# Kernel tuning notes

Hardware: AMD Instinct MI355X
Metric: run time of the kernel (lower is better)

The kernel has to match this reference:

```python
import jax, jax.numpy as jnp
import numpy as np

H = 16  # num_heads

def setup_inputs() -> dict:
    key = jax.random.key(0)
    k1, k2, k3 = jax.random.split(key, 3)
    D = 1024
    x = jax.random.normal(k1, (4, 2048, D), dtype=jnp.float32)
    W_qkv = jax.random.normal(k2, (D, 3 * D), dtype=jnp.float32) * (1.0 / np.sqrt(D))
    b_qkv = jnp.zeros((3 * D,), dtype=jnp.float32)
    W_out = jax.random.normal(k3, (D, D), dtype=jnp.float32) * (1.0 / np.sqrt(D))
    b_out = jnp.zeros((D,), dtype=jnp.float32)
    return {"x": x, "W_qkv": W_qkv, "b_qkv": b_qkv, "W_out": W_out, "b_out": b_out}

def reference(x, W_qkv, b_qkv, W_out, b_out):
    B, S, D = x.shape
    hd = D // H  # head_dim
    qkv = x @ W_qkv + b_qkv  # [B,S,3D]
    q, k, v = jnp.split(qkv, 3, axis=-1)
    # [B,S,D] -> [B,H,S,hd]
    q = q.reshape(B, S, H, hd).transpose(0, 2, 1, 3)
    k = k.reshape(B, S, H, hd).transpose(0, 2, 1, 3)
    v = v.reshape(B, S, H, hd).transpose(0, 2, 1, 3)
    scores = jnp.einsum('bhqd,bhkd->bhqk', q, k) / jnp.sqrt(jnp.float32(hd))
    weights = jax.nn.softmax(scores, axis=-1)  # dropout p=0.0 (eval)
    out = jnp.einsum('bhqk,bhkd->bhqd', weights, v)
    out = out.transpose(0, 2, 1, 3).reshape(B, S, D)
    return out @ W_out + b_out
```

## Files before the change

kernel.cpp:

```cpp
#include <hip/hip_runtime.h>

typedef __bf16 bf16;
typedef __bf16 bf16x8 __attribute__((ext_vector_type(8)));
typedef float f32x4 __attribute__((ext_vector_type(4)));
typedef unsigned u32x2 __attribute__((ext_vector_type(2)));

static constexpr int NB = 4;
static constexpr int NS = 2048;
static constexpr int ND = 1024;
static constexpr int NH = 16;
static constexpr int HD = 64;
static constexpr float QSCALE = 0.18033688011112042f;

#define GL16(g, l)                                                             \
    __builtin_amdgcn_global_load_lds(                                          \
        (const __attribute__((address_space(1))) void*)(g),                    \
        (__attribute__((address_space(3))) void*)(l), 16, 0, 0)

static __device__ __forceinline__ unsigned pk2(float a, float b) {
    union { __bf16 h[2]; unsigned u; } t;
    t.h[0] = (__bf16)a; t.h[1] = (__bf16)b;
    return t.u;
}

__global__ void k_conv(const float* __restrict__ in, bf16* __restrict__ out, int n) {
    int i = (blockIdx.x * blockDim.x + threadIdx.x) * 4;
    if (i < n) {
        float4 v = *reinterpret_cast<const float4*>(in + i);
        bf16* o = out + i;
        o[0] = (bf16)v.x; o[1] = (bf16)v.y; o[2] = (bf16)v.z; o[3] = (bf16)v.w;
    }
}

__global__ void k_transconv(const float* __restrict__ in, bf16* __restrict__ out,
                            int K, int N) {
    __shared__ float tile[32][33];
    int k0 = blockIdx.y * 32, n0 = blockIdx.x * 32;
    int tx = threadIdx.x, ty = threadIdx.y;
    for (int j = 0; j < 32; j += 8)
        tile[ty + j][tx] = in[(long)(k0 + ty + j) * N + n0 + tx];
    __syncthreads();
    for (int j = 0; j < 32; j += 8)
        out[(long)(n0 + ty + j) * K + k0 + tx] = (bf16)tile[tx][ty + j];
}

template <int EPI>
__global__ __launch_bounds__(256, 2) void k_gemm(
    const bf16* __restrict__ A, const bf16* __restrict__ Bt,
    const float* __restrict__ bias,
    void* __restrict__ out0, void* __restrict__ out1, void* __restrict__ out2,
    int M, int N, int Kd)
{
    constexpr int BM = 128, BN = 128, BK = 64;
    __shared__ __align__(16) bf16 As[2][BM * BK];
    __shared__ __align__(16) bf16 Bs[2][BN * BK];

    const int t = threadIdx.x;
    const int wid = t >> 6, lane = t & 63;
    const int wm = wid >> 1, wn = wid & 1;
    const int m0 = blockIdx.y * BM, n0 = blockIdx.x * BN;
    const int lrow = lane & 15, lhi = lane >> 4;

    const int srow0 = wid * 32 + (lane >> 3);
    const int scol = ((lane & 7) ^ (lane >> 3)) * 8;
    const bf16* ag = A + (long)(m0 + srow0) * Kd + scol;
    const bf16* bg = Bt + (long)(n0 + srow0) * Kd + scol;

    auto STAGE = [&](int buf_, int k0_) {
#pragma unroll
        for (int c = 0; c < 4; ++c) {
            GL16(ag + (long)(c * 8) * Kd + k0_, &As[buf_][(wid * 32 + c * 8) * BK]);
            GL16(bg + (long)(c * 8) * Kd + k0_, &Bs[buf_][(wid * 32 + c * 8) * BK]);
        }
    };

    f32x4 acc[4][4] = {};
    const int nt = Kd >> 6;
    const int swzr = (lrow & 7) << 4;
    int co[2];
#pragma unroll
    for (int kk = 0; kk < 2; ++kk)
        co[kk] = ((kk * 64 + lhi * 16) ^ swzr) >> 1;

    STAGE(0, 0);
    int cur = 0;
    for (int tix = 0; tix < nt; ++tix) {
        if (tix + 1 < nt) {
            STAGE(cur ^ 1, (tix + 1) * BK);
            asm volatile("s_waitcnt vmcnt(8)" ::: "memory");
        } else {
            asm volatile("s_waitcnt vmcnt(0)" ::: "memory");
        }
        __builtin_amdgcn_s_barrier();
        __builtin_amdgcn_sched_barrier(0);

        bf16x8 af[2][4], bfr[2][4];
#pragma unroll
        for (int kk = 0; kk < 2; ++kk)
#pragma unroll
            for (int i = 0; i < 4; ++i) {
                af[kk][i]  = *reinterpret_cast<const bf16x8*>(
                    &As[cur][(wm * 64 + i * 16 + lrow) * BK + co[kk]]);
                bfr[kk][i] = *reinterpret_cast<const bf16x8*>(
                    &Bs[cur][(wn * 64 + i * 16 + lrow) * BK + co[kk]]);
            }
        __builtin_amdgcn_s_setprio(1);
#pragma unroll
        for (int kk = 0; kk < 2; ++kk)
#pragma unroll
            for (int i = 0; i < 4; ++i)
#pragma unroll
                for (int j = 0; j < 4; ++j)
                    acc[i][j] = __builtin_amdgcn_mfma_f32_16x16x32_bf16(
                        af[kk][i], bfr[kk][j], acc[i][j], 0, 0, 0);
        __builtin_amdgcn_s_setprio(0);
        __builtin_amdgcn_s_barrier();
        cur ^= 1;
    }

    if (EPI == 0) {
        bf16* Qb = (bf16*)out0; bf16* Kb = (bf16*)out1; bf16* Vt = (bf16*)out2;
#pragma unroll
        for (int j = 0; j < 4; ++j) {
            int col = n0 + wn * 64 + j * 16 + lrow;
            float bv = bias[col];
            int which = col >> 10;
            int rem = col & 1023;
            int h = rem >> 6, d = rem & 63;
#pragma unroll
            for (int i = 0; i < 4; ++i) {
                int mbase = m0 + wm * 64 + i * 16 + lhi * 4;
#pragma unroll
                for (int r = 0; r < 4; ++r) {
                    int row = mbase + r;
                    int bb = row >> 11, s = row & 2047;
                    long bh = bb * NH + h;
                    float v = acc[i][j][r] + bv;
                    if (which == 0)      Qb[(bh * NS + s) * HD + d] = (bf16)(v * QSCALE);
                    else if (which == 1) Kb[(bh * NS + s) * HD + d] = (bf16)v;
                    else                 Vt[(bh * HD + d) * NS + s] = (bf16)v;
                }
            }
        }
    } else {
        float* O = (float*)out0;
#pragma unroll
        for (int j = 0; j < 4; ++j) {
            int col = n0 + wn * 64 + j * 16 + lrow;
            float bv = bias[col];
#pragma unroll
            for (int i = 0; i < 4; ++i) {
                int mbase = m0 + wm * 64 + i * 16 + lhi * 4;
#pragma unroll
                for (int r = 0; r < 4; ++r)
                    O[(long)(mbase + r) * N + col] = acc[i][j][r] + bv;
            }
        }
    }
}

__global__ __launch_bounds__(256, 4) void k_attn(
    const bf16* __restrict__ Qb, const bf16* __restrict__ Kb,
    const bf16* __restrict__ Vt, bf16* __restrict__ Ao)
{
    constexpr int KB = 64;
    constexpr int NT = NS / KB;
    __shared__ __align__(16) bf16 Ks[2][KB * HD];
    __shared__ __align__(16) bf16 Vs[2][HD * KB];
    __shared__ __align__(16) bf16 Ps[4 * 16 * 64];

    const int t = threadIdx.x;
    const int wid = t >> 6, lane = t & 63;
    const int lrow = lane & 15, lhi = lane >> 4;

    const int flat = blockIdx.y * gridDim.x + blockIdx.x;
    const int n = (flat & 7) * 128 + (flat >> 3);
    const int bh = n >> 4;
    const int qw = (n & 15) * 128 + wid * 32;

    const bf16* Qg = Qb + ((long)bh * NS + qw) * HD;
    const bf16* Kg = Kb + (long)bh * NS * HD;
    const bf16* Vg = Vt + (long)bh * HD * NS;

    bf16x8 qf[2][2];
#pragma unroll
    for (int qfr = 0; qfr < 2; ++qfr)
#pragma unroll
        for (int c = 0; c < 2; ++c)
            qf[qfr][c] = *reinterpret_cast<const bf16x8*>(
                Qg + (long)(qfr * 16 + lrow) * HD + c * 32 + lhi * 8);

    f32x4 of[2][4] = {};
    float lsum[2] = {0.f, 0.f};

    const int gsr = lane >> 3;
    const int gsc = ((lane & 7) ^ gsr) * 8;
    auto STAGE = [&](int buf, int kb) {
#pragma unroll
        for (int c = 0; c < 2; ++c) {
            const int rb = wid * 16 + c * 8;
            GL16(Kg + (long)(kb + rb + gsr) * HD + gsc, &Ks[buf][rb * 64]);
            GL16(Vg + (long)(rb + gsr) * NS + kb + gsc, &Vs[buf][rb * 64]);
        }
    };

    const int rsw = (lrow & 7) << 4;
    bf16* psw = &Ps[wid * 1024 + lrow * 64];

    auto COMPUTE = [&](int b_) {
        f32x4 st[2][4] = {};
        __builtin_amdgcn_s_setprio(1);
#pragma unroll
        for (int j = 0; j < 4; ++j)
#pragma unroll
            for (int c = 0; c < 2; ++c) {
                bf16x8 kf = *reinterpret_cast<const bf16x8*>(
                    &Ks[b_][(j * 16 + lrow) * 64 + (((c * 64 + lhi * 16) ^ rsw) >> 1)]);
#pragma unroll
                for (int qfr = 0; qfr < 2; ++qfr)
                    st[qfr][j] = __builtin_amdgcn_mfma_f32_16x16x32_bf16(
                        kf, qf[qfr][c], st[qfr][j], 0, 0, 0);
            }
        __builtin_amdgcn_s_setprio(0);

        bf16x8 pfr[2][2];
#pragma unroll
        for (int qfr = 0; qfr < 2; ++qfr) {
#pragma unroll
            for (int j = 0; j < 4; ++j) {
                float e0 = __builtin_amdgcn_exp2f(st[qfr][j][0]);
                float e1 = __builtin_amdgcn_exp2f(st[qfr][j][1]);
                float e2 = __builtin_amdgcn_exp2f(st[qfr][j][2]);
                float e3 = __builtin_amdgcn_exp2f(st[qfr][j][3]);
                lsum[qfr] += (e0 + e1) + (e2 + e3);
                u32x2 w; w[0] = pk2(e0, e1); w[1] = pk2(e2, e3);
                *reinterpret_cast<u32x2*>(
                    reinterpret_cast<char*>(psw) + (((j * 32 + lhi * 8) ^ rsw))) = w;
            }
            asm volatile("" ::: "memory");
#pragma unroll
            for (int chunk = 0; chunk < 2; ++chunk)
                pfr[qfr][chunk] = *reinterpret_cast<const bf16x8*>(
                    reinterpret_cast<char*>(psw) + ((chunk * 64 + lhi * 16) ^ rsw));
            asm volatile("" ::: "memory");
        }

        __builtin_amdgcn_s_setprio(1);
#pragma unroll
        for (int chunk = 0; chunk < 2; ++chunk)
#pragma unroll
            for (int f = 0; f < 4; ++f) {
                bf16x8 vf = *reinterpret_cast<const bf16x8*>(
                    &Vs[b_][(f * 16 + lrow) * 64 +
                            (((chunk * 64 + lhi * 16) ^ rsw) >> 1)]);
#pragma unroll
                for (int qfr = 0; qfr < 2; ++qfr)
                    of[qfr][f] = __builtin_amdgcn_mfma_f32_16x16x32_bf16(
                        pfr[qfr][chunk], vf, of[qfr][f], 0, 0, 0);
            }
        __builtin_amdgcn_s_setprio(0);
    };

    STAGE(0, 0);
    int cur = 0;
    for (int it = 0; it < NT; ++it) {
        if (it + 1 < NT) {
            STAGE(cur ^ 1, (it + 1) * KB);
            asm volatile("s_waitcnt vmcnt(4)" ::: "memory");
        } else {
            asm volatile("s_waitcnt vmcnt(0)" ::: "memory");
        }
        __builtin_amdgcn_s_barrier();
        __builtin_amdgcn_sched_barrier(0);
        COMPUTE(cur);
        __builtin_amdgcn_s_barrier();
        cur ^= 1;
    }

#pragma unroll
    for (int qfr = 0; qfr < 2; ++qfr) {
        lsum[qfr] += __shfl_xor(lsum[qfr], 16);
        lsum[qfr] += __shfl_xor(lsum[qfr], 32);
    }

    const int bb = bh >> 4, h = bh & 15;
#pragma unroll
    for (int qfr = 0; qfr < 2; ++qfr) {
#pragma unroll
        for (int r = 0; r < 4; ++r) {
            float inv = 1.0f / __shfl(lsum[qfr], 4 * lhi + r);
            int s = qw + qfr * 16 + 4 * lhi + r;
#pragma unroll
            for (int f = 0; f < 4; ++f)
                Ao[((long)bb * NS + s) * ND + h * HD + f * 16 + lrow] =
                    (bf16)(of[qfr][f][r] * inv);
        }
    }
}

extern "C" void kernel_launch(void* const* d_in, const int* in_sizes, int n_in,
                              void* d_out, int out_size, void* d_ws, size_t ws_size,
                              hipStream_t stream) {
    const float* x    = (const float*)d_in[0];
    const float* Wqkv = (const float*)d_in[1];
    const float* bqkv = (const float*)d_in[2];
    const float* Wout = (const float*)d_in[3];
    const float* bout = (const float*)d_in[4];
    float* out = (float*)d_out;

    char* ws = (char*)d_ws;
    bf16* Xb  = (bf16*)(ws);
    bf16* Wqt = (bf16*)(ws + 16777216);
    bf16* Wot = (bf16*)(ws + 23068672);
    bf16* Qb  = (bf16*)(ws + 25165824);
    bf16* Kb  = (bf16*)(ws + 41943040);
    bf16* Vt  = (bf16*)(ws + 58720256);
    bf16* Ab  = (bf16*)(ws + 75497472);

    k_conv<<<dim3(8192), dim3(256), 0, stream>>>(x, Xb, NB * NS * ND);
    k_transconv<<<dim3(96, 32), dim3(32, 8), 0, stream>>>(Wqkv, Wqt, ND, 3 * ND);
    k_transconv<<<dim3(32, 32), dim3(32, 8), 0, stream>>>(Wout, Wot, ND, ND);

    k_gemm<0><<<dim3(24, 64), dim3(256), 0, stream>>>(
        Xb, Wqt, bqkv, Qb, Kb, Vt, NB * NS, 3 * ND, ND);

    k_attn<<<dim3(16, 64), dim3(256), 0, stream>>>(Qb, Kb, Vt, Ab);

    k_gemm<1><<<dim3(8, 64), dim3(256), 0, stream>>>(
        Ab, Wot, bout, out, nullptr, nullptr, NB * NS, ND, ND);
}
```

Measured before the change: 219.5 us.

## Enlarge GEMM tile to 256x128 with 8 waves and split-phase A staging

The projection GEMMs move from 128x128 tiles with 4 waves to 256x128 tiles with 8 waves, halving the number of M-blocks. Each K iteration is split into two halves: the first half of the next A tile and the B tile are staged before the first MFMA block, and the second half of A is staged after it. This lets global loads overlap compute, and B fragments are reused across both halves. The intent is better B reuse per block and finer-grained overlap of memory with MFMA. The cost is larger LDS use and more waves per block, and the wait counts must match the number of loads in flight exactly.

```diff
diff --git a/kernel.cpp b/kernel.cpp
--- a/kernel.cpp
+++ b/kernel.cpp
@@ -45,97 +45,135 @@
 }
 
 template <int EPI>
-__global__ __launch_bounds__(256, 2) void k_gemm(
+__global__ __launch_bounds__(512, 2) void k_gemm(
     const bf16* __restrict__ A, const bf16* __restrict__ Bt,
     const float* __restrict__ bias,
     void* __restrict__ out0, void* __restrict__ out1, void* __restrict__ out2,
     int M, int N, int Kd)
 {
-    constexpr int BM = 128, BN = 128, BK = 64;
+    constexpr int BM = 256, BN = 128, BK = 64;
     __shared__ __align__(16) bf16 As[2][BM * BK];
     __shared__ __align__(16) bf16 Bs[2][BN * BK];
 
     const int t = threadIdx.x;
     const int wid = t >> 6, lane = t & 63;
-    const int wm = wid >> 1, wn = wid & 1;
+    const int wr = wid >> 1, wc = wid & 1;
     const int m0 = blockIdx.y * BM, n0 = blockIdx.x * BN;
     const int lrow = lane & 15, lhi = lane >> 4;
 
-    const int srow0 = wid * 32 + (lane >> 3);
-    const int scol = ((lane & 7) ^ (lane >> 3)) * 8;
-    const bf16* ag = A + (long)(m0 + srow0) * Kd + scol;
-    const bf16* bg = Bt + (long)(n0 + srow0) * Kd + scol;
-
-    auto STAGE = [&](int buf_, int k0_) {
-#pragma unroll
-        for (int c = 0; c < 4; ++c) {
-            GL16(ag + (long)(c * 8) * Kd + k0_, &As[buf_][(wid * 32 + c * 8) * BK]);
-            GL16(bg + (long)(c * 8) * Kd + k0_, &Bs[buf_][(wid * 32 + c * 8) * BK]);
-        }
+    const int slr = lane >> 3;
+    const int scol = ((lane & 7) ^ slr) * 8;
+    const int g0 = wid * 2, g1 = wid * 2 + 1;
+    const int aR0 = (g0 >> 2) * 64 + (g0 & 3) * 8;
+    const int aR1 = (g1 >> 2) * 64 + (g1 & 3) * 8;
+    const int bR0 = g0 * 8, bR1 = g1 * 8;
+
+    auto STAGE_A = [&](int buf, int kb, int h) {
+        GL16(A + (long)(m0 + aR0 + h * 32 + slr) * Kd + kb + scol,
+             &As[buf][(aR0 + h * 32) * BK]);
+        GL16(A + (long)(m0 + aR1 + h * 32 + slr) * Kd + kb + scol,
+             &As[buf][(aR1 + h * 32) * BK]);
+    };
+    auto STAGE_B = [&](int buf, int kb) {
+        GL16(Bt + (long)(n0 + bR0 + slr) * Kd + kb + scol, &Bs[buf][bR0 * BK]);
+        GL16(Bt + (long)(n0 + bR1 + slr) * Kd + kb + scol, &Bs[buf][bR1 * BK]);
     };
 
     f32x4 acc[4][4] = {};
     const int nt = Kd >> 6;
-    const int swzr = (lrow & 7) << 4;
+    const int swz = (lrow & 7) << 4;
     int co[2];
 #pragma unroll
     for (int kk = 0; kk < 2; ++kk)
-        co[kk] = ((kk * 64 + lhi * 16) ^ swzr) >> 1;
-
-    STAGE(0, 0);
-    int cur = 0;
-    for (int tix = 0; tix < nt; ++tix) {
-        if (tix + 1 < nt) {
-            STAGE(cur ^ 1, (tix + 1) * BK);
-            asm volatile("s_waitcnt vmcnt(8)" ::: "memory");
+        co[kk] = ((kk * 64 + lhi * 16) ^ swz) >> 1;
+
+    STAGE_A(0, 0, 0);
+    STAGE_B(0, 0);
+    STAGE_A(0, 0, 1);
+
+    bf16x8 bfr[4][2];
+    for (int t2 = 0; t2 < nt; ++t2) {
+        const int buf = t2 & 1, nbuf = buf ^ 1;
+        const int kb1 = (t2 + 1) * BK;
+        if (t2 + 1 < nt) {
+            STAGE_A(nbuf, kb1, 0);
+            STAGE_B(nbuf, kb1);
+            asm volatile("s_waitcnt vmcnt(6)" ::: "memory");
+        } else {
+            asm volatile("s_waitcnt vmcnt(2)" ::: "memory");
+        }
+        __builtin_amdgcn_s_barrier();
+        __builtin_amdgcn_sched_barrier(0);
+
+        bf16x8 af[2][2];
+#pragma unroll
+        for (int nj = 0; nj < 4; ++nj)
+#pragma unroll
+            for (int kk = 0; kk < 2; ++kk)
+                bfr[nj][kk] = *reinterpret_cast<const bf16x8*>(
+                    &Bs[buf][(wc * 64 + nj * 16 + lrow) * BK + co[kk]]);
+#pragma unroll
+        for (int mi = 0; mi < 2; ++mi)
+#pragma unroll
+            for (int kk = 0; kk < 2; ++kk)
+                af[mi][kk] = *reinterpret_cast<const bf16x8*>(
+                    &As[buf][(wr * 64 + mi * 16 + lrow) * BK + co[kk]]);
+        __builtin_amdgcn_s_setprio(1);
+#pragma unroll
+        for (int kk = 0; kk < 2; ++kk)
+#pragma unroll
+            for (int mi = 0; mi < 2; ++mi)
+#pragma unroll
+                for (int nj = 0; nj < 4; ++nj)
+                    acc[mi][nj] = __builtin_amdgcn_mfma_f32_16x16x32_bf16(
+                        af[mi][kk], bfr[nj][kk], acc[mi][nj], 0, 0, 0);
+        __builtin_amdgcn_s_setprio(0);
+
+        if (t2 + 1 < nt) {
+            STAGE_A(nbuf, kb1, 1);
+            asm volatile("s_waitcnt vmcnt(6)" ::: "memory");
         } else {
             asm volatile("s_waitcnt vmcnt(0)" ::: "memory");
         }
         __builtin_amdgcn_s_barrier();
         __builtin_amdgcn_sched_barrier(0);
 
-        bf16x8 af[2][4], bfr[2][4];
+#pragma unroll
+        for (int mi = 0; mi < 2; ++mi)
+#pragma unroll
+            for (int kk = 0; kk < 2; ++kk)
+                af[mi][kk] = *reinterpret_cast<const bf16x8*>(
+                    &As[buf][(wr * 64 + 32 + mi * 16 + lrow) * BK + co[kk]]);
+        __builtin_amdgcn_s_setprio(1);
 #pragma unroll
         for (int kk = 0; kk < 2; ++kk)
 #pragma unroll
-            for (int i = 0; i < 4; ++i) {
-                af[kk][i]  = *reinterpret_cast<const bf16x8*>(
-                    &As[cur][(wm * 64 + i * 16 + lrow) * BK + co[kk]]);
-                bfr[kk][i] = *reinterpret_cast<const bf16x8*>(
-                    &Bs[cur][(wn * 64 + i * 16 + lrow) * BK + co[kk]]);
-            }
-        __builtin_amdgcn_s_setprio(1);
-#pragma unroll
-        for (int kk = 0; kk < 2; ++kk)
-#pragma unroll
-            for (int i = 0; i < 4; ++i)
-#pragma unroll
-                for (int j = 0; j < 4; ++j)
-                    acc[i][j] = __builtin_amdgcn_mfma_f32_16x16x32_bf16(
-                        af[kk][i], bfr[kk][j], acc[i][j], 0, 0, 0);
+            for (int mi = 0; mi < 2; ++mi)
+#pragma unroll
+                for (int nj = 0; nj < 4; ++nj)
+                    acc[2 + mi][nj] = __builtin_amdgcn_mfma_f32_16x16x32_bf16(
+                        af[mi][kk], bfr[nj][kk], acc[2 + mi][nj], 0, 0, 0);
         __builtin_amdgcn_s_setprio(0);
-        __builtin_amdgcn_s_barrier();
-        cur ^= 1;
     }
 
     if (EPI == 0) {
         bf16* Qb = (bf16*)out0; bf16* Kb = (bf16*)out1; bf16* Vt = (bf16*)out2;
 #pragma unroll
-        for (int j = 0; j < 4; ++j) {
-            int col = n0 + wn * 64 + j * 16 + lrow;
+        for (int nj = 0; nj < 4; ++nj) {
+            int col = n0 + wc * 64 + nj * 16 + lrow;
             float bv = bias[col];
             int which = col >> 10;
             int rem = col & 1023;
             int h = rem >> 6, d = rem & 63;
 #pragma unroll
-            for (int i = 0; i < 4; ++i) {
-                int mbase = m0 + wm * 64 + i * 16 + lhi * 4;
+            for (int mi = 0; mi < 4; ++mi) {
+                int mbase = m0 + wr * 64 + mi * 16 + lhi * 4;
 #pragma unroll
                 for (int r = 0; r < 4; ++r) {
                     int row = mbase + r;
                     int bb = row >> 11, s = row & 2047;
                     long bh = bb * NH + h;
-                    float v = acc[i][j][r] + bv;
+                    float v = acc[mi][nj][r] + bv;
                     if (which == 0)      Qb[(bh * NS + s) * HD + d] = (bf16)(v * QSCALE);
                     else if (which == 1) Kb[(bh * NS + s) * HD + d] = (bf16)v;
                     else                 Vt[(bh * HD + d) * NS + s] = (bf16)v;
@@ -145,15 +183,15 @@
     } else {
         float* O = (float*)out0;
 #pragma unroll
-        for (int j = 0; j < 4; ++j) {
-            int col = n0 + wn * 64 + j * 16 + lrow;
+        for (int nj = 0; nj < 4; ++nj) {
+            int col = n0 + wc * 64 + nj * 16 + lrow;
             float bv = bias[col];
 #pragma unroll
-            for (int i = 0; i < 4; ++i) {
-                int mbase = m0 + wm * 64 + i * 16 + lhi * 4;
+            for (int mi = 0; mi < 4; ++mi) {
+                int mbase = m0 + wr * 64 + mi * 16 + lhi * 4;
 #pragma unroll
                 for (int r = 0; r < 4; ++r)
-                    O[(long)(mbase + r) * N + col] = acc[i][j][r] + bv;
+                    O[(long)(mbase + r) * N + col] = acc[mi][nj][r] + bv;
             }
         }
     }
@@ -321,11 +359,11 @@
     k_transconv<<<dim3(96, 32), dim3(32, 8), 0, stream>>>(Wqkv, Wqt, ND, 3 * ND);
     k_transconv<<<dim3(32, 32), dim3(32, 8), 0, stream>>>(Wout, Wot, ND, ND);
 
-    k_gemm<0><<<dim3(24, 64), dim3(256), 0, stream>>>(
+    k_gemm<0><<<dim3(24, 32), dim3(512), 0, stream>>>(
         Xb, Wqt, bqkv, Qb, Kb, Vt, NB * NS, 3 * ND, ND);
 
     k_attn<<<dim3(16, 64), dim3(256), 0, stream>>>(Qb, Kb, Vt, Ab);
 
-    k_gemm<1><<<dim3(8, 64), dim3(256), 0, stream>>>(
+    k_gemm<1><<<dim3(8, 32), dim3(512), 0, stream>>>(
         Ab, Wot, bout, out, nullptr, nullptr, NB * NS, ND, ND);
 }
```

After: 233.1 us. +6.2%, slower.

## Use 256x256 tile, 8-wave GEMM with phased LDS reads for QKV projection

Applied to the files above, without the earlier changes.

Replaces the 128x128, 4-wave QKV projection GEMM with a dedicated kernel using 256x256 block tiles and 512 threads. Each wave computes a 128x64 sub-tile in four phases, interleaving LDS fragment loads with MFMA bursts under explicit waitcnt, barriers and setprio. The larger tile raises arithmetic intensity per LDS byte and cuts global traffic for the QKV GEMM. In exchange it uses more registers and LDS, launches fewer blocks (384), and adds more barriers per K step.

```diff
diff --git a/kernel.cpp b/kernel.cpp
--- a/kernel.cpp
+++ b/kernel.cpp
@@ -44,11 +44,177 @@
         out[(long)(n0 + ty + j) * K + k0 + tx] = (bf16)tile[tx][ty + j];
 }
 
-template <int EPI>
-__global__ __launch_bounds__(256, 2) void k_gemm(
+__global__ __launch_bounds__(512, 2) void k_gemmA(
     const bf16* __restrict__ A, const bf16* __restrict__ Bt,
     const float* __restrict__ bias,
-    void* __restrict__ out0, void* __restrict__ out1, void* __restrict__ out2,
+    bf16* __restrict__ Qb, bf16* __restrict__ Kb, bf16* __restrict__ Vt,
+    int M, int N, int Kd)
+{
+    constexpr int BK = 64;
+    __shared__ __align__(16) bf16 As[2][2][128 * BK];
+    __shared__ __align__(16) bf16 Bs[2][2][128 * BK];
+
+    const int t = threadIdx.x;
+    const int wid = t >> 6, lane = t & 63;
+    const int wr = wid >> 2;
+    const int wc = wid & 3;
+    const int wcH = wc >> 1;
+    const int m0 = blockIdx.y * 256, n0 = blockIdx.x * 256;
+    const int lrow = lane & 15, lhi = lane >> 4;
+
+    const int slr = lane >> 3;
+    const int scol = ((lane & 7) ^ slr) * 8;
+    const int arow = (wid & 3) * 32;
+    const int bg = (wid & 1) | ((wid >> 2) << 1);
+    const int brow = bg * 32;
+
+    auto STAGE8 = [&](int buf, int kt) {
+        const long kb = (long)kt * BK;
+#pragma unroll
+        for (int u = 0; u < 4; ++u)
+            GL16(A + (long)(m0 + wr * 128 + arow + u * 8 + slr) * Kd + kb + scol,
+                 &As[buf][wr][(arow + u * 8) * BK]);
+#pragma unroll
+        for (int u = 0; u < 4; ++u)
+            GL16(Bt + (long)(n0 + wcH * 128 + brow + u * 8 + slr) * Kd + kb + scol,
+                 &Bs[buf][wcH][(brow + u * 8) * BK]);
+    };
+
+    f32x4 acc[8][4] = {};
+    const int nt = Kd >> 6;
+    const int swz = (lrow & 7) << 4;
+    int co[2];
+#pragma unroll
+    for (int kk = 0; kk < 2; ++kk)
+        co[kk] = ((kk * 64 + lhi * 16) ^ swz) >> 1;
+
+    const bf16* asb;
+    const bf16* bsb;
+
+    STAGE8(0, 0);
+
+    bf16x8 bfr[4][2];
+    bf16x8 af[4][2];
+
+    for (int kt = 0; kt < nt; ++kt) {
+        const int buf = kt & 1;
+        if (kt + 1 < nt) {
+            STAGE8(buf ^ 1, kt + 1);
+            asm volatile("s_waitcnt vmcnt(8)" ::: "memory");
+        } else {
+            asm volatile("s_waitcnt vmcnt(0)" ::: "memory");
+        }
+        __builtin_amdgcn_s_barrier();
+        __builtin_amdgcn_sched_barrier(0);
+        asb = &As[buf][wr][0];
+        bsb = &Bs[buf][wcH][0];
+
+#pragma unroll
+        for (int nj = 0; nj < 2; ++nj)
+#pragma unroll
+            for (int kk = 0; kk < 2; ++kk)
+                bfr[nj][kk] = *reinterpret_cast<const bf16x8*>(
+                    &bsb[((wc & 1) * 64 + nj * 16 + lrow) * BK + co[kk]]);
+#pragma unroll
+        for (int i = 0; i < 4; ++i)
+#pragma unroll
+            for (int kk = 0; kk < 2; ++kk)
+                af[i][kk] = *reinterpret_cast<const bf16x8*>(
+                    &asb[(i * 16 + lrow) * BK + co[kk]]);
+        asm volatile("s_waitcnt lgkmcnt(0)" ::: "memory");
+        __builtin_amdgcn_sched_barrier(0);
+        __builtin_amdgcn_s_setprio(1);
+#pragma unroll
+        for (int kk = 0; kk < 2; ++kk)
+#pragma unroll
+            for (int i = 0; i < 4; ++i)
+#pragma unroll
+                for (int nj = 0; nj < 2; ++nj)
+                    acc[i][nj] = __builtin_amdgcn_mfma_f32_16x16x32_bf16(
+                        af[i][kk], bfr[nj][kk], acc[i][nj], 0, 0, 0);
+        __builtin_amdgcn_s_setprio(0);
+        __builtin_amdgcn_s_barrier();
+
+#pragma unroll
+        for (int nj = 2; nj < 4; ++nj)
+#pragma unroll
+            for (int kk = 0; kk < 2; ++kk)
+                bfr[nj][kk] = *reinterpret_cast<const bf16x8*>(
+                    &bsb[((wc & 1) * 64 + nj * 16 + lrow) * BK + co[kk]]);
+        asm volatile("s_waitcnt lgkmcnt(0)" ::: "memory");
+        __builtin_amdgcn_sched_barrier(0);
+        __builtin_amdgcn_s_setprio(1);
+#pragma unroll
+        for (int kk = 0; kk < 2; ++kk)
+#pragma unroll
+            for (int i = 0; i < 4; ++i)
+#pragma unroll
+                for (int nj = 2; nj < 4; ++nj)
+                    acc[i][nj] = __builtin_amdgcn_mfma_f32_16x16x32_bf16(
+                        af[i][kk], bfr[nj][kk], acc[i][nj], 0, 0, 0);
+        __builtin_amdgcn_s_setprio(0);
+        __builtin_amdgcn_s_barrier();
+
+#pragma unroll
+        for (int i = 0; i < 4; ++i)
+#pragma unroll
+            for (int kk = 0; kk < 2; ++kk)
+                af[i][kk] = *reinterpret_cast<const bf16x8*>(
+                    &asb[(64 + i * 16 + lrow) * BK + co[kk]]);
+        asm volatile("s_waitcnt lgkmcnt(0)" ::: "memory");
+        __builtin_amdgcn_sched_barrier(0);
+        __builtin_amdgcn_s_setprio(1);
+#pragma unroll
+        for (int kk = 0; kk < 2; ++kk)
+#pragma unroll
+            for (int i = 0; i < 4; ++i)
+#pragma unroll
+                for (int nj = 0; nj < 2; ++nj)
+                    acc[4 + i][nj] = __builtin_amdgcn_mfma_f32_16x16x32_bf16(
+                        af[i][kk], bfr[nj][kk], acc[4 + i][nj], 0, 0, 0);
+        __builtin_amdgcn_s_setprio(0);
+        __builtin_amdgcn_s_barrier();
+
+        __builtin_amdgcn_s_setprio(1);
+#pragma unroll
+        for (int kk = 0; kk < 2; ++kk)
+#pragma unroll
+            for (int i = 0; i < 4; ++i)
+#pragma unroll
+                for (int nj = 2; nj < 4; ++nj)
+                    acc[4 + i][nj] = __builtin_amdgcn_mfma_f32_16x16x32_bf16(
+                        af[i][kk], bfr[nj][kk], acc[4 + i][nj], 0, 0, 0);
+        __builtin_amdgcn_s_setprio(0);
+        __builtin_amdgcn_s_barrier();
+    }
+
+#pragma unroll
+    for (int nj = 0; nj < 4; ++nj) {
+        int col = n0 + wc * 64 + nj * 16 + lrow;
+        float bv = bias[col];
+        int which = col >> 10;
+        int rem = col & 1023;
+        int h = rem >> 6, d = rem & 63;
+#pragma unroll
+        for (int mi = 0; mi < 8; ++mi) {
+            int mbase = m0 + wr * 128 + mi * 16 + lhi * 4;
+#pragma unroll
+            for (int r = 0; r < 4; ++r) {
+                int row = mbase + r;
+                int bb = row >> 11, s = row & 2047;
+                long bh = bb * NH + h;
+                float v = acc[mi][nj][r] + bv;
+                if (which == 0)      Qb[(bh * NS + s) * HD + d] = (bf16)(v * QSCALE);
+                else if (which == 1) Kb[(bh * NS + s) * HD + d] = (bf16)v;
+                else                 Vt[(bh * HD + d) * NS + s] = (bf16)v;
+            }
+        }
+    }
+}
+
+__global__ __launch_bounds__(256, 2) void k_gemmB(
+    const bf16* __restrict__ A, const bf16* __restrict__ Bt,
+    const float* __restrict__ bias, float* __restrict__ O,
     int M, int N, int Kd)
 {
     constexpr int BM = 128, BN = 128, BK = 64;
@@ -118,43 +284,16 @@
         cur ^= 1;
     }
 
-    if (EPI == 0) {
-        bf16* Qb = (bf16*)out0; bf16* Kb = (bf16*)out1; bf16* Vt = (bf16*)out2;
-#pragma unroll
-        for (int j = 0; j < 4; ++j) {
-            int col = n0 + wn * 64 + j * 16 + lrow;
-            float bv = bias[col];
-            int which = col >> 10;
-            int rem = col & 1023;
-            int h = rem >> 6, d = rem & 63;
-#pragma unroll
-            for (int i = 0; i < 4; ++i) {
-                int mbase = m0 + wm * 64 + i * 16 + lhi * 4;
-#pragma unroll
-                for (int r = 0; r < 4; ++r) {
-                    int row = mbase + r;
-                    int bb = row >> 11, s = row & 2047;
-                    long bh = bb * NH + h;
-                    float v = acc[i][j][r] + bv;
-                    if (which == 0)      Qb[(bh * NS + s) * HD + d] = (bf16)(v * QSCALE);
-                    else if (which == 1) Kb[(bh * NS + s) * HD + d] = (bf16)v;
-                    else                 Vt[(bh * HD + d) * NS + s] = (bf16)v;
-                }
-            }
-        }
-    } else {
-        float* O = (float*)out0;
-#pragma unroll
-        for (int j = 0; j < 4; ++j) {
-            int col = n0 + wn * 64 + j * 16 + lrow;
-            float bv = bias[col];
-#pragma unroll
-            for (int i = 0; i < 4; ++i) {
-                int mbase = m0 + wm * 64 + i * 16 + lhi * 4;
-#pragma unroll
-                for (int r = 0; r < 4; ++r)
-                    O[(long)(mbase + r) * N + col] = acc[i][j][r] + bv;
-            }
+#pragma unroll
+    for (int j = 0; j < 4; ++j) {
+        int col = n0 + wn * 64 + j * 16 + lrow;
+        float bv = bias[col];
+#pragma unroll
+        for (int i = 0; i < 4; ++i) {
+            int mbase = m0 + wm * 64 + i * 16 + lhi * 4;
+#pragma unroll
+            for (int r = 0; r < 4; ++r)
+                O[(long)(mbase + r) * N + col] = acc[i][j][r] + bv;
         }
     }
 }
@@ -321,11 +460,11 @@
     k_transconv<<<dim3(96, 32), dim3(32, 8), 0, stream>>>(Wqkv, Wqt, ND, 3 * ND);
     k_transconv<<<dim3(32, 32), dim3(32, 8), 0, stream>>>(Wout, Wot, ND, ND);
 
-    k_gemm<0><<<dim3(24, 64), dim3(256), 0, stream>>>(
+    k_gemmA<<<dim3(12, 32), dim3(512), 0, stream>>>(
         Xb, Wqt, bqkv, Qb, Kb, Vt, NB * NS, 3 * ND, ND);
 
     k_attn<<<dim3(16, 64), dim3(256), 0, stream>>>(Qb, Kb, Vt, Ab);
 
-    k_gemm<1><<<dim3(8, 64), dim3(256), 0, stream>>>(
-        Ab, Wot, bout, out, nullptr, nullptr, NB * NS, ND, ND);
-}
+    k_gemmB<<<dim3(8, 64), dim3(256), 0, stream>>>(
+        Ab, Wot, bout, out, NB * NS, ND, ND);
+}
```

After: 239.1 us. +9.0%, slower.

## Stage GEMM and attention epilogues through LDS for vectorized coalesced stores

Applied to the files above, without the earlier changes.

Rewrites the QKV, output-projection and attention epilogues so that accumulators are first written into swizzled LDS and then stored to global memory as contiguous 16-byte vectors. Before, each thread issued scattered 2-byte or 4-byte stores. The Q/K and V projections are split into two launches. The V launch swaps the MFMA operands so its tile comes out transposed, making the Vt writes contiguous along the sequence. The attention PV MFMA operands are also swapped to give a layout suited to row-major staging. The cost is extra LDS round trips, reuse of the operand buffers after the main loop, and one more kernel launch.

```diff
diff --git a/kernel.cpp b/kernel.cpp
--- a/kernel.cpp
+++ b/kernel.cpp
@@ -1,6 +1,7 @@
 #include <hip/hip_runtime.h>
 
 typedef __bf16 bf16;
+typedef __bf16 bf16x4 __attribute__((ext_vector_type(4)));
 typedef __bf16 bf16x8 __attribute__((ext_vector_type(8)));
 typedef float f32x4 __attribute__((ext_vector_type(4)));
 typedef unsigned u32x2 __attribute__((ext_vector_type(2)));
@@ -44,12 +45,12 @@
         out[(long)(n0 + ty + j) * K + k0 + tx] = (bf16)tile[tx][ty + j];
 }
 
-template <int EPI>
+template <int MODE>
 __global__ __launch_bounds__(256, 2) void k_gemm(
     const bf16* __restrict__ A, const bf16* __restrict__ Bt,
     const float* __restrict__ bias,
-    void* __restrict__ out0, void* __restrict__ out1, void* __restrict__ out2,
-    int M, int N, int Kd)
+    void* __restrict__ out0, void* __restrict__ out1,
+    int M, int Kd)
 {
     constexpr int BM = 128, BN = 128, BK = 64;
     __shared__ __align__(16) bf16 As[2][BM * BK];
@@ -110,51 +111,113 @@
 #pragma unroll
             for (int i = 0; i < 4; ++i)
 #pragma unroll
-                for (int j = 0; j < 4; ++j)
-                    acc[i][j] = __builtin_amdgcn_mfma_f32_16x16x32_bf16(
-                        af[kk][i], bfr[kk][j], acc[i][j], 0, 0, 0);
+                for (int j = 0; j < 4; ++j) {
+                    if (MODE == 1)
+                        acc[i][j] = __builtin_amdgcn_mfma_f32_16x16x32_bf16(
+                            af[kk][i], bfr[kk][j], acc[i][j], 0, 0, 0);
+                    else
+                        acc[i][j] = __builtin_amdgcn_mfma_f32_16x16x32_bf16(
+                            bfr[kk][j], af[kk][i], acc[i][j], 0, 0, 0);
+                }
         __builtin_amdgcn_s_setprio(0);
         __builtin_amdgcn_s_barrier();
         cur ^= 1;
     }
 
-    if (EPI == 0) {
-        bf16* Qb = (bf16*)out0; bf16* Kb = (bf16*)out1; bf16* Vt = (bf16*)out2;
+    const int colbase = n0 + wn * 64;
+
+    if (MODE == 0) {
+        bf16* eb = (bf16*)As + wid * 4096;
+        const bool isQ = (colbase >> 10) == 0;
 #pragma unroll
         for (int j = 0; j < 4; ++j) {
-            int col = n0 + wn * 64 + j * 16 + lrow;
-            float bv = bias[col];
-            int which = col >> 10;
-            int rem = col & 1023;
-            int h = rem >> 6, d = rem & 63;
+            f32x4 bv = *reinterpret_cast<const f32x4*>(&bias[colbase + j * 16 + 4 * lhi]);
 #pragma unroll
             for (int i = 0; i < 4; ++i) {
-                int mbase = m0 + wm * 64 + i * 16 + lhi * 4;
+                int srt = i * 16 + lrow;
+                bf16x4 pk;
 #pragma unroll
                 for (int r = 0; r < 4; ++r) {
-                    int row = mbase + r;
-                    int bb = row >> 11, s = row & 2047;
-                    long bh = bb * NH + h;
-                    float v = acc[i][j][r] + bv;
-                    if (which == 0)      Qb[(bh * NS + s) * HD + d] = (bf16)(v * QSCALE);
-                    else if (which == 1) Kb[(bh * NS + s) * HD + d] = (bf16)v;
-                    else                 Vt[(bh * HD + d) * NS + s] = (bf16)v;
+                    float v = acc[i][j][r] + bv[r];
+                    pk[r] = (bf16)(isQ ? v * QSCALE : v);
                 }
-            }
+                *reinterpret_cast<bf16x4*>(
+                    reinterpret_cast<char*>(eb) + srt * 128 +
+                    (((j * 16 + 4 * lhi) * 2) ^ ((srt & 7) << 4))) = pk;
+            }
+        }
+        const int h = (colbase & 1023) >> 6;
+        bf16* Ob = isQ ? (bf16*)out0 : (bf16*)out1;
+#pragma unroll
+        for (int it = 0; it < 8; ++it) {
+            int rt = it * 8 + (lane >> 3);
+            bf16x8 v = *reinterpret_cast<const bf16x8*>(
+                reinterpret_cast<char*>(eb) + rt * 128 +
+                (((lane & 7) * 16) ^ ((rt & 7) << 4)));
+            int row = m0 + wm * 64 + rt;
+            int bb = row >> 11, s = row & 2047;
+            long bh = (long)bb * NH + h;
+            *reinterpret_cast<bf16x8*>(&Ob[(bh * NS + s) * HD + (lane & 7) * 8]) = v;
+        }
+    } else if (MODE == 1) {
+        bf16* eb = (bf16*)As + wid * 4096;
+#pragma unroll
+        for (int j = 0; j < 4; ++j) {
+            float bv = bias[colbase + j * 16 + lrow];
+            int drt = j * 16 + lrow;
+#pragma unroll
+            for (int i = 0; i < 4; ++i) {
+                bf16x4 pk;
+#pragma unroll
+                for (int r = 0; r < 4; ++r) pk[r] = (bf16)(acc[i][j][r] + bv);
+                *reinterpret_cast<bf16x4*>(
+                    reinterpret_cast<char*>(eb) + drt * 128 +
+                    (((i * 16 + 4 * lhi) * 2) ^ ((drt & 7) << 4))) = pk;
+            }
+        }
+        const int h = (colbase & 1023) >> 6;
+        const int mrow = m0 + wm * 64;
+        const int bb = mrow >> 11, s0 = mrow & 2047;
+        bf16* Vt = (bf16*)out0;
+#pragma unroll
+        for (int it = 0; it < 8; ++it) {
+            int dt = it * 8 + (lane >> 3);
+            bf16x8 v = *reinterpret_cast<const bf16x8*>(
+                reinterpret_cast<char*>(eb) + dt * 128 +
+                (((lane & 7) * 16) ^ ((dt & 7) << 4)));
+            long bh = (long)bb * NH + h;
+            *reinterpret_cast<bf16x8*>(&Vt[(bh * HD + dt) * NS + s0 + (lane & 7) * 8]) = v;
         }
     } else {
+        float* ef = (float*)As + wid * 2048;
         float* O = (float*)out0;
 #pragma unroll
-        for (int j = 0; j < 4; ++j) {
-            int col = n0 + wn * 64 + j * 16 + lrow;
-            float bv = bias[col];
-#pragma unroll
-            for (int i = 0; i < 4; ++i) {
-                int mbase = m0 + wm * 64 + i * 16 + lhi * 4;
-#pragma unroll
-                for (int r = 0; r < 4; ++r)
-                    O[(long)(mbase + r) * N + col] = acc[i][j][r] + bv;
-            }
+        for (int half = 0; half < 2; ++half) {
+#pragma unroll
+            for (int i2 = 0; i2 < 2; ++i2) {
+                int i = half * 2 + i2;
+                int srt = i2 * 16 + lrow;
+#pragma unroll
+                for (int j = 0; j < 4; ++j) {
+                    f32x4 bv = *reinterpret_cast<const f32x4*>(
+                        &bias[colbase + j * 16 + 4 * lhi]);
+                    f32x4 v = acc[i][j] + bv;
+                    *reinterpret_cast<f32x4*>(
+                        reinterpret_cast<char*>(ef) + srt * 256 +
+                        (((j * 16 + 4 * lhi) * 4) ^ ((srt & 7) << 4))) = v;
+                }
+            }
+#pragma unroll
+            for (int it = 0; it < 8; ++it) {
+                int rt = it * 4 + (lane >> 4);
+                f32x4 v = *reinterpret_cast<const f32x4*>(
+                    reinterpret_cast<char*>(ef) + rt * 256 +
+                    (((lane & 15) * 16) ^ ((rt & 7) << 4)));
+                int row = m0 + wm * 64 + half * 32 + rt;
+                *reinterpret_cast<f32x4*>(
+                    &O[(long)row * 1024 + colbase + (lane & 15) * 4]) = v;
+            }
+            asm volatile("" ::: "memory");
         }
     }
 }
@@ -256,7 +319,7 @@
 #pragma unroll
                 for (int qfr = 0; qfr < 2; ++qfr)
                     of[qfr][f] = __builtin_amdgcn_mfma_f32_16x16x32_bf16(
-                        pfr[qfr][chunk], vf, of[qfr][f], 0, 0, 0);
+                        vf, pfr[qfr][chunk], of[qfr][f], 0, 0, 0);
             }
         __builtin_amdgcn_s_setprio(0);
     };
@@ -283,18 +346,31 @@
         lsum[qfr] += __shfl_xor(lsum[qfr], 32);
     }
 
+    bf16* eb = (bf16*)Ks + wid * 2048;
+#pragma unroll
+    for (int qfr = 0; qfr < 2; ++qfr) {
+        float inv = 1.0f / lsum[qfr];
+        int srt = qfr * 16 + lrow;
+#pragma unroll
+        for (int f = 0; f < 4; ++f) {
+            bf16x4 pk;
+#pragma unroll
+            for (int r = 0; r < 4; ++r) pk[r] = (bf16)(of[qfr][f][r] * inv);
+            *reinterpret_cast<bf16x4*>(
+                reinterpret_cast<char*>(eb) + srt * 128 +
+                (((f * 16 + 4 * lhi) * 2) ^ ((srt & 7) << 4))) = pk;
+        }
+    }
     const int bb = bh >> 4, h = bh & 15;
 #pragma unroll
-    for (int qfr = 0; qfr < 2; ++qfr) {
-#pragma unroll
-        for (int r = 0; r < 4; ++r) {
-            float inv = 1.0f / __shfl(lsum[qfr], 4 * lhi + r);
-            int s = qw + qfr * 16 + 4 * lhi + r;
-#pragma unroll
-            for (int f = 0; f < 4; ++f)
-                Ao[((long)bb * NS + s) * ND + h * HD + f * 16 + lrow] =
-                    (bf16)(of[qfr][f][r] * inv);
-        }
+    for (int it = 0; it < 4; ++it) {
+        int rt = it * 8 + (lane >> 3);
+        bf16x8 v = *reinterpret_cast<const bf16x8*>(
+            reinterpret_cast<char*>(eb) + rt * 128 +
+            (((lane & 7) * 16) ^ ((rt & 7) << 4)));
+        int s = qw + rt;
+        *reinterpret_cast<bf16x8*>(
+            &Ao[((long)bb * NS + s) * ND + h * HD + (lane & 7) * 8]) = v;
     }
 }
 
@@ -321,11 +397,13 @@
     k_transconv<<<dim3(96, 32), dim3(32, 8), 0, stream>>>(Wqkv, Wqt, ND, 3 * ND);
     k_transconv<<<dim3(32, 32), dim3(32, 8), 0, stream>>>(Wout, Wot, ND, ND);
 
-    k_gemm<0><<<dim3(24, 64), dim3(256), 0, stream>>>(
-        Xb, Wqt, bqkv, Qb, Kb, Vt, NB * NS, 3 * ND, ND);
+    k_gemm<0><<<dim3(16, 64), dim3(256), 0, stream>>>(
+        Xb, Wqt, bqkv, Qb, Kb, NB * NS, ND);
+    k_gemm<1><<<dim3(8, 64), dim3(256), 0, stream>>>(
+        Xb, Wqt + (long)2048 * ND, bqkv + 2048, Vt, nullptr, NB * NS, ND);
 
     k_attn<<<dim3(16, 64), dim3(256), 0, stream>>>(Qb, Kb, Vt, Ab);
 
-    k_gemm<1><<<dim3(8, 64), dim3(256), 0, stream>>>(
-        Ab, Wot, bout, out, nullptr, nullptr, NB * NS, ND, ND);
-}
+    k_gemm<2><<<dim3(8, 64), dim3(256), 0, stream>>>(
+        Ab, Wot, bout, out, nullptr, NB * NS, ND);
+}
```

After: 199.3 us. 1.1x faster.
